# Optimization experiments

Measured on AMD Instinct MI355X. Metric: run time of the kernel, lower is better.

## Reference

```python
import jax, jax.numpy as jnp
import numpy as np

B, N, D = 2, 4096, 2048
H, DH, W = 8, 128, 512          # heads (num_queries), dim_head, window_size
SCALE = 8.0                      # qk_scale (qk_rmsnorm=True)


def setup_inputs() -> dict:
    key = jax.random.key(0)
    ks = jax.random.split(key, 5)
    return {
        "x": jax.random.normal(ks[0], (B, N, D), jnp.float32),
        "Wq": jax.random.normal(ks[1], (H * DH, D), jnp.float32) * 0.02,
        "Wkv": jax.random.normal(ks[2], (2 * H * DH, D), jnp.float32) * 0.02,
        "q_scale": jnp.ones((DH,), jnp.float32),
        "k_scale": jnp.ones((DH,), jnp.float32),
        "Wg": jax.random.normal(ks[3], (H, D), jnp.float32) * 0.02,
        "bg": jnp.zeros((H,), jnp.float32),
        "Wo": jax.random.normal(ks[4], (D, H * DH), jnp.float32) * 0.02,
    }


def _l2norm(t):
    # F.normalize: x / max(||x||, eps)
    return t / jnp.maximum(jnp.linalg.norm(t, axis=-1, keepdims=True), 1e-12)


def reference(x, Wq, Wkv, q_scale, k_scale, Wg, bg, Wo):
    b, n, _ = x.shape
    inner = H * DH
    q = (x @ Wq.T).reshape(b, n, H, DH).transpose(0, 2, 1, 3)      # b h n d
    kv = x @ Wkv.T
    k = kv[..., :inner].reshape(b, n, H, DH).transpose(0, 2, 1, 3)
    v = kv[..., inner:].reshape(b, n, H, DH).transpose(0, 2, 1, 3)
    # qk rmsnorm
    q = _l2norm(q) * q_scale
    k = _l2norm(k) * k_scale

    nb = n // W
    qb = q.reshape(b, H, nb, W, DH)
    kb = k.reshape(b, H, nb, W, DH)
    vb = v.reshape(b, H, nb, W, DH)

    def look_around(t):  # prepend previous bucket (look_backward=1)
        prev = jnp.concatenate([jnp.zeros_like(t[:, :, :1]), t[:, :, :-1]], axis=2)
        return jnp.concatenate([prev, t], axis=3)  # b h nb 2W d

    kw, vw = look_around(kb), look_around(vb)

    pos = jnp.arange(n).reshape(nb, W)
    pos_prev = jnp.concatenate([jnp.full((1, W), -1), pos[:-1]], axis=0)
    posk = jnp.concatenate([pos_prev, pos], axis=1)                 # nb 2W
    dist = pos[:, :, None] - posk[:, None, :]                       # nb W 2W
    # causal + exact window: attend j with 0 <= i - j <= W, valid (non-pad) key
    mask = (posk[:, None, :] >= 0) & (dist >= 0) & (dist <= W)

    sim = jnp.einsum('bhnid,bhnjd->bhnij', qb * SCALE, kw)
    sim = jnp.where(mask, sim, jnp.finfo(sim.dtype).min)
    attn = jax.nn.softmax(sim, axis=-1)
    o = jnp.einsum('bhnij,bhnjd->bhnid', attn, vw).reshape(b, H, n, DH)

    # per-head sigmoid value gating
    gates = jax.nn.sigmoid(jnp.einsum('bnd,hd->bhn', x, Wg) + bg[None, :, None])
    o = o * gates[..., None]

    o = o.transpose(0, 2, 1, 3).reshape(b, n, inner)                # b n (h d)
    return o @ Wo.T
```

## Files before the change

### kernel.cpp

```cpp
#include <hip/hip_runtime.h>
#include <hip/hip_bf16.h>
#include <cstdint>

typedef short short8 __attribute__((ext_vector_type(8)));
typedef __bf16 bf16x8 __attribute__((ext_vector_type(8)));
typedef float f32x4 __attribute__((ext_vector_type(4)));
typedef unsigned short u16;
typedef unsigned int u32;

#define B_  2
#define N_  4096
#define D_  2048
#define H_  8
#define DH_ 128
#define W_  512
#define M_  (B_*N_)
#define INNER_ (H_*DH_)

static __device__ __forceinline__ u16 f2bf(float f) {
  u32 u = __float_as_uint(f);
  u32 r = (u + 0x7fffu + ((u >> 16) & 1u)) >> 16;
  return (u16)r;
}
static __device__ __forceinline__ float bf2f(u16 u) {
  return __uint_as_float(((u32)u) << 16);
}
static __device__ __forceinline__ f32x4 mfma16(short8 a, short8 b, f32x4 c) {
  return __builtin_amdgcn_mfma_f32_16x16x32_bf16(
      __builtin_bit_cast(bf16x8, a), __builtin_bit_cast(bf16x8, b), c, 0, 0, 0);
}

#define GLOAD_LDS16(g, s) \
  __builtin_amdgcn_global_load_lds((const __attribute__((address_space(1))) void*)(g), \
                                   (__attribute__((address_space(3))) void*)(s), 16, 0, 0)

__global__ __launch_bounds__(256) void cvt_kernel(
    const float* __restrict__ x, const float* __restrict__ Wq,
    const float* __restrict__ Wkv, const float* __restrict__ Wo,
    u16* __restrict__ xb, u16* __restrict__ Wcat, u16* __restrict__ Wob) {
  size_t i = ((size_t)blockIdx.x * 256 + threadIdx.x) * 8;
  const float* src; u16* dst; size_t off;
  const size_t SX = 16777216ul, SQ = 2097152ul, SKV = 4194304ul;
  if (i < SX)                { src = x;   dst = xb;             off = i; }
  else if (i < SX+SQ)        { src = Wq;  dst = Wcat;           off = i - SX; }
  else if (i < SX+SQ+SKV)    { src = Wkv; dst = Wcat + 2097152; off = i - SX - SQ; }
  else                       { src = Wo;  dst = Wob;            off = i - SX - SQ - SKV; }
  float4 a = *(const float4*)(src + off);
  float4 b = *(const float4*)(src + off + 4);
  short8 o;
  o[0]=(short)f2bf(a.x); o[1]=(short)f2bf(a.y); o[2]=(short)f2bf(a.z); o[3]=(short)f2bf(a.w);
  o[4]=(short)f2bf(b.x); o[5]=(short)f2bf(b.y); o[6]=(short)f2bf(b.z); o[7]=(short)f2bf(b.w);
  *(short8*)(dst + off) = o;
}

#define BARRIER() __builtin_amdgcn_s_barrier()
#define WAIT_LGKM0() do { asm volatile("s_waitcnt lgkmcnt(0)" ::: "memory"); \
                          __builtin_amdgcn_sched_barrier(0); } while(0)
#define WVM8 asm volatile("s_waitcnt vmcnt(8)" ::: "memory")
#define WVM4 asm volatile("s_waitcnt vmcnt(4)" ::: "memory")
#define WVM0 asm volatile("s_waitcnt vmcnt(0)" ::: "memory")
#define WNONE ((void)0)

#define STAGE_HALF(gbase, sreg) do { \
    const u16* _g = (gbase) + _cs; \
    GLOAD_LDS16(_g + (size_t)(wv*32 + (lane>>2))*K,      (sreg) + wv*1024); \
    GLOAD_LDS16(_g + (size_t)(wv*32 + 16 + (lane>>2))*K, (sreg) + wv*1024 + 512); \
  } while(0)

#define LOAD_AF(sreg, mfb) do { \
    _Pragma("unroll") for (int q = 0; q < 4; ++q) \
      af[q] = *(const short8*)((sreg) + (wm*128 + ((mfb)+q)*16 + l15)*32 + fch); \
  } while(0)
#define LOAD_BF(sreg) do { \
    _Pragma("unroll") for (int q = 0; q < 4; ++q) \
      bf[q] = *(const short8*)((sreg) + (wn*64 + q*16 + l15)*32 + fch); \
  } while(0)

#define PH_MFMA(mfb) do { \
    __builtin_amdgcn_s_setprio(1); \
    _Pragma("unroll") for (int q = 0; q < 4; ++q) \
      _Pragma("unroll") for (int nf = 0; nf < 4; ++nf) \
        acc[(mfb)+q][nf] = mfma16(af[q], bf[nf], acc[(mfb)+q][nf]); \
    __builtin_amdgcn_s_setprio(0); \
  } while(0)

#define TILE4(T, SA_C, SB_C, SA_N, SB_N, C1, C2, WB, WA) do { \
    const u16* gAt = gA + (size_t)(T)*64; \
    const u16* gBt = gB + (size_t)(T)*64; \
    short8 af[4], bf[4]; \
    LOAD_AF(SA_C, 0); LOAD_BF(SB_C); \
    if (C1) STAGE_HALF(gAt + 96, (SA_N) + 8192); \
    BARRIER(); WAIT_LGKM0(); PH_MFMA(0); BARRIER(); \
    LOAD_AF(SA_C, 4); \
    if (C1) STAGE_HALF(gBt + 96, (SB_N) + 8192); \
    WB; \
    BARRIER(); WAIT_LGKM0(); PH_MFMA(4); BARRIER(); \
    LOAD_AF((SA_C) + 8192, 0); LOAD_BF((SB_C) + 8192); \
    if (C2) STAGE_HALF(gAt + 128, SA_C); \
    BARRIER(); WAIT_LGKM0(); PH_MFMA(0); BARRIER(); \
    LOAD_AF((SA_C) + 8192, 4); \
    if (C2) STAGE_HALF(gBt + 128, SB_C); \
    WA; \
    BARRIER(); WAIT_LGKM0(); PH_MFMA(4); BARRIER(); \
  } while(0)

template<int EPI>
__global__ __launch_bounds__(512, 2) void gemm256(
    const u16* __restrict__ A, const u16* __restrict__ Bw,
    u16* __restrict__ Dq, u16* __restrict__ Dk, u16* __restrict__ Dv,
    float* __restrict__ Cf, int Ncols, int K) {
  extern __shared__ u16 lds[];
  const int tid = threadIdx.x;
  const int lane = tid & 63, wv = tid >> 6;
  const int wm = wv >> 2, wn = wv & 3;
  const int l15 = lane & 15, l4 = lane >> 4;

  const int nwg = gridDim.x;
  const int swz = (blockIdx.x & 7) * (nwg >> 3) + (blockIdx.x >> 3);
  const int by = swz & 31;
  const int bx = swz >> 5;
  const int m0 = by << 8, n0 = bx << 8;

  const u16* gA = A + (size_t)m0 * K;
  const u16* gB = Bw + (size_t)n0 * K;
  u16* sA0 = lds;
  u16* sB0 = lds + 32768;

  const int _cs = ((lane & 3) ^ ((lane >> 3) & 3)) * 8;
  const int fch = (l4 ^ ((l15 >> 1) & 3)) * 8;

  f32x4 acc[8][4] = {};

  STAGE_HALF(gA,      sA0);
  STAGE_HALF(gB,      sB0);
  STAGE_HALF(gA + 32, sA0 + 8192);
  STAGE_HALF(gB + 32, sB0 + 8192);
  STAGE_HALF(gA + 64, sA0 + 16384);
  STAGE_HALF(gB + 64, sB0 + 16384);
  WVM4;
  BARRIER();

  const int nt = K >> 6;
  #pragma unroll 1
  for (int t = 0; t < nt - 2; t += 2) {
    TILE4(t,     sA0,         sB0,         sA0 + 16384, sB0 + 16384, true, true, WVM8, WVM8);
    TILE4(t + 1, sA0 + 16384, sB0 + 16384, sA0,         sB0,         true, true, WVM8, WVM8);
  }
  TILE4(nt - 2, sA0,         sB0,         sA0 + 16384, sB0 + 16384, true,  false, WVM8, WVM4);
  TILE4(nt - 1, sA0 + 16384, sB0 + 16384, sA0,         sB0,         false, false, WVM0, WNONE);

  if (EPI == 0) {
    #pragma unroll
    for (int mf = 0; mf < 8; ++mf)
      #pragma unroll
      for (int nf = 0; nf < 4; ++nf)
        #pragma unroll
        for (int j = 0; j < 4; ++j) {
          int m = m0 + wm*128 + mf*16 + l4*4 + j;
          int gc = n0 + wn*64 + nf*16 + l15;
          int bufsel = gc >> 10, inner = gc & 1023, h = inner >> 7, d = inner & 127;
          u16* dst = bufsel == 0 ? Dq : (bufsel == 1 ? Dk : Dv);
          int b = m >> 12, n = m & (N_ - 1);
          dst[(((size_t)(b*H_ + h)*N_ + n) << 7) + d] = f2bf(acc[mf][nf][j]);
        }
  } else {
    #pragma unroll
    for (int mf = 0; mf < 8; ++mf)
      #pragma unroll
      for (int nf = 0; nf < 4; ++nf)
        #pragma unroll
        for (int j = 0; j < 4; ++j) {
          int m = m0 + wm*128 + mf*16 + l4*4 + j;
          int gc = n0 + wn*64 + nf*16 + l15;
          Cf[(size_t)m*Ncols + gc] = acc[mf][nf][j];
        }
  }
}

__global__ __launch_bounds__(256) void normqk_kernel(
    u16* __restrict__ qb, u16* __restrict__ kb,
    const float* __restrict__ qs, const float* __restrict__ ks) {
  int lane = threadIdx.x & 63, wv = threadIdx.x >> 6;
  size_t vec = (size_t)blockIdx.x * 4 + wv;
  bool isq = vec < 65536;
  u16* p = isq ? qb + vec*128 : kb + (vec - 65536)*128;
  const float* sc = isq ? qs : ks;
  u32 u = *(const u32*)(p + lane*2);
  float a = bf2f((u16)(u & 0xffffu));
  float b = bf2f((u16)(u >> 16));
  float ss = a*a + b*b;
  #pragma unroll
  for (int off = 32; off >= 1; off >>= 1) ss += __shfl_xor(ss, off);
  float inv = 1.0f / fmaxf(sqrtf(ss), 1e-12f);
  if (isq) inv *= 8.0f;
  float r0 = a * inv * sc[lane*2];
  float r1 = b * inv * sc[lane*2 + 1];
  *(u32*)(p + lane*2) = (u32)f2bf(r0) | ((u32)f2bf(r1) << 16);
}

__global__ __launch_bounds__(256) void transpose_v_kernel(
    const u16* __restrict__ v, u16* __restrict__ vT) {
  int bh = blockIdx.x >> 6;
  int n0 = (blockIdx.x & 63) << 6;
  __shared__ u16 tl[64][136];
  int tid = threadIdx.x;
  #pragma unroll
  for (int r = 0; r < 4; ++r) {
    int cf = r*256 + tid;
    int row = cf >> 4, ch = cf & 15;
    *(short8*)&tl[row][ch*8] = *(const short8*)(v + ((size_t)bh*N_ + n0 + row)*128 + ch*8);
  }
  __syncthreads();
  #pragma unroll
  for (int r = 0; r < 4; ++r) {
    int cf = r*256 + tid;
    int d = cf >> 3, nch = cf & 7;
    short8 o;
    #pragma unroll
    for (int i = 0; i < 8; ++i) o[i] = (short)tl[nch*8 + i][d];
    *(short8*)(vT + ((size_t)bh*128 + d)*N_ + n0 + nch*8) = o;
  }
}

__global__ __launch_bounds__(256) void gates_kernel(
    const float* __restrict__ x, const float* __restrict__ Wg,
    const float* __restrict__ bg, float* __restrict__ gates) {
  int m = blockIdx.x;
  int tid = threadIdx.x;
  const float* xr = x + (size_t)m * D_;
  float acc[8] = {};
  for (int d = tid; d < D_; d += 256) {
    float xv = xr[d];
    #pragma unroll
    for (int h = 0; h < 8; ++h) acc[h] = fmaf(xv, Wg[h*D_ + d], acc[h]);
  }
  #pragma unroll
  for (int h = 0; h < 8; ++h)
    #pragma unroll
    for (int off = 32; off >= 1; off >>= 1) acc[h] += __shfl_xor(acc[h], off);
  __shared__ float red[4][8];
  int lane = tid & 63, wv = tid >> 6;
  if (lane == 0) {
    #pragma unroll
    for (int h = 0; h < 8; ++h) red[wv][h] = acc[h];
  }
  __syncthreads();
  if (tid < 8) {
    float vsum = red[0][tid] + red[1][tid] + red[2][tid] + red[3][tid] + bg[tid];
    gates[(size_t)m*8 + tid] = 1.0f / (1.0f + __expf(-vsum));
  }
}

__global__ __launch_bounds__(256) void attn_kernel(
    const u16* __restrict__ q, const u16* __restrict__ k,
    const u16* __restrict__ vT, const float* __restrict__ gates,
    u16* __restrict__ o) {
  const int bid = blockIdx.x;
  const int t = bid & 3;
  const int c = (bid >> 2) & 7;
  const int bh = bid >> 5;
  const int b = bh >> 3, h = bh & 7;
  const int i0 = c*W_ + t*128;
  const int tid = threadIdx.x;
  const int lane = tid & 63, wv = tid >> 6;
  const int l15 = lane & 15, l4 = lane >> 4;

  __shared__ u16 sK[64*128];
  __shared__ u16 sV[128*64];
  __shared__ u16 sP[4][32*64];

  short8 qf[2][4];
  const u16* qbase = q + (((size_t)bh*N_ + i0 + wv*32) << 7);
  #pragma unroll
  for (int mf = 0; mf < 2; ++mf)
    #pragma unroll
    for (int ks = 0; ks < 4; ++ks)
      qf[mf][ks] = *(const short8*)(qbase + (mf*16 + l15)*128 + ks*32 + l4*8);

  float mrow[2][4], lrow[2][4];
  f32x4 oacc[2][8];
  #pragma unroll
  for (int mf = 0; mf < 2; ++mf) {
    #pragma unroll
    for (int j = 0; j < 4; ++j) { mrow[mf][j] = -1e30f; lrow[mf][j] = 0.f; }
    #pragma unroll
    for (int df = 0; df < 8; ++df) oacc[mf][df] = (f32x4){0.f,0.f,0.f,0.f};
  }
  u16* sPw = &sP[wv][0];

  #pragma unroll 1
  for (int kt = 0; kt < 10; ++kt) {
    const int j0 = i0 - 512 + kt*64;
    if (j0 < 0) continue;
    __syncthreads();
    #pragma unroll
    for (int r = 0; r < 4; ++r) {
      int cf = r*256 + tid;
      int row = cf >> 4, cph = cf & 15;
      int clg = cph ^ (row & 15);
      GLOAD_LDS16(k + (((size_t)bh*N_ + j0 + row) << 7) + clg*8, sK + (size_t)(r*256 + wv*64)*8);
    }
    #pragma unroll
    for (int r = 0; r < 4; ++r) {
      int cf = r*256 + tid;
      int row = cf >> 3, cph = cf & 7;
      int clg = cph ^ (row & 7);
      GLOAD_LDS16(vT + ((size_t)bh*128 + row)*N_ + j0 + clg*8, sV + (size_t)(r*256 + wv*64)*8);
    }
    __syncthreads();

    f32x4 s[2][4];
    #pragma unroll
    for (int mf = 0; mf < 2; ++mf)
      #pragma unroll
      for (int nf = 0; nf < 4; ++nf) s[mf][nf] = (f32x4){0.f,0.f,0.f,0.f};
    #pragma unroll
    for (int ks = 0; ks < 4; ++ks) {
      short8 kb[4];
      #pragma unroll
      for (int nf = 0; nf < 4; ++nf) {
        int row = nf*16 + l15;
        int ch = (ks*4 + l4) ^ (row & 15);
        kb[nf] = *(const short8*)(sK + row*128 + ch*8);
      }
      #pragma unroll
      for (int mf = 0; mf < 2; ++mf)
        #pragma unroll
        for (int nf = 0; nf < 4; ++nf)
          s[mf][nf] = mfma16(qf[mf][ks], kb[nf], s[mf][nf]);
    }

    if (kt < 2 || kt > 7) {
      #pragma unroll
      for (int mf = 0; mf < 2; ++mf)
        #pragma unroll
        for (int nf = 0; nf < 4; ++nf)
          #pragma unroll
          for (int j = 0; j < 4; ++j) {
            int r = wv*32 + mf*16 + l4*4 + j;
            int sidx = nf*16 + l15;
            int dist = (i0 + r) - (j0 + sidx);
            if (dist < 0 || dist > 512) s[mf][nf][j] = -1e30f;
          }
    }

    #pragma unroll
    for (int mf = 0; mf < 2; ++mf) {
      #pragma unroll
      for (int j = 0; j < 4; ++j) {
        float mx = fmaxf(fmaxf(s[mf][0][j], s[mf][1][j]), fmaxf(s[mf][2][j], s[mf][3][j]));
        #pragma unroll
        for (int off = 1; off <= 8; off <<= 1) mx = fmaxf(mx, __shfl_xor(mx, off));
        float mnew = fmaxf(mrow[mf][j], mx);
        float scal = __expf(mrow[mf][j] - mnew);
        mrow[mf][j] = mnew;
        float ls = 0.f;
        #pragma unroll
        for (int nf = 0; nf < 4; ++nf) {
          float p = __expf(s[mf][nf][j] - mnew);
          s[mf][nf][j] = p;
          ls += p;
        }
        #pragma unroll
        for (int off = 1; off <= 8; off <<= 1) ls += __shfl_xor(ls, off);
        lrow[mf][j] = lrow[mf][j]*scal + ls;
        #pragma unroll
        for (int df = 0; df < 8; ++df) oacc[mf][df][j] *= scal;
        int prow = mf*16 + l4*4 + j;
        #pragma unroll
        for (int nf = 0; nf < 4; ++nf) {
          int pcol = nf*16 + l15;
          int ch = (pcol >> 3) ^ (prow & 7);
          sPw[prow*64 + ch*8 + (pcol & 7)] = f2bf(s[mf][nf][j]);
        }
      }
    }

    #pragma unroll
    for (int ks2 = 0; ks2 < 2; ++ks2) {
      short8 pa[2];
      #pragma unroll
      for (int mf = 0; mf < 2; ++mf) {
        int prow = mf*16 + l15;
        int ch = (ks2*4 + l4) ^ (prow & 7);
        pa[mf] = *(const short8*)(sPw + prow*64 + ch*8);
      }
      #pragma unroll
      for (int df = 0; df < 8; ++df) {
        int vd = df*16 + l15;
        int ch2 = (ks2*4 + l4) ^ (vd & 7);
        short8 vb = *(const short8*)(sV + vd*64 + ch2*8);
        #pragma unroll
        for (int mf = 0; mf < 2; ++mf)
          oacc[mf][df] = mfma16(pa[mf], vb, oacc[mf][df]);
      }
    }
  }

  #pragma unroll
  for (int mf = 0; mf < 2; ++mf)
    #pragma unroll
    for (int j = 0; j < 4; ++j) {
      int r = wv*32 + mf*16 + l4*4 + j;
      int i = i0 + r;
      float f = (1.0f / lrow[mf][j]) * gates[((size_t)b*N_ + i)*8 + h];
      #pragma unroll
      for (int df = 0; df < 8; ++df)
        o[((size_t)b*N_ + i)*INNER_ + h*128 + df*16 + l15] = f2bf(oacc[mf][df][j] * f);
    }
}

extern "C" void kernel_launch(void* const* d_in, const int* in_sizes, int n_in,
                              void* d_out, int out_size, void* d_ws, size_t ws_size,
                              hipStream_t stream) {
  const float* x       = (const float*)d_in[0];
  const float* Wq      = (const float*)d_in[1];
  const float* Wkv     = (const float*)d_in[2];
  const float* q_scale = (const float*)d_in[3];
  const float* k_scale = (const float*)d_in[4];
  const float* Wg      = (const float*)d_in[5];
  const float* bg      = (const float*)d_in[6];
  const float* Wo      = (const float*)d_in[7];
  float* out = (float*)d_out;

  u16* qb  = (u16*)d_out;
  u16* kb  = qb + 8388608;
  u16* vb  = kb + 8388608;
  u16* vTb = vb + 8388608;

  char* w = (char*)d_ws;
  u16* xb   = (u16*)w;
  u16* ob   = (u16*)w;
  u16* Wcat = (u16*)(w + 33554432);
  u16* Wob  = (u16*)(w + 46137344);
  float* gb = (float*)(w + 50331648);
  (void)in_sizes; (void)n_in; (void)out_size; (void)ws_size;

  hipFuncSetAttribute((const void*)gemm256<0>,
                      hipFuncAttributeMaxDynamicSharedMemorySize, 131072);
  hipFuncSetAttribute((const void*)gemm256<1>,
                      hipFuncAttributeMaxDynamicSharedMemorySize, 131072);

  cvt_kernel<<<12288, 256, 0, stream>>>(x, Wq, Wkv, Wo, xb, Wcat, Wob);
  gemm256<0><<<384, 512, 131072, stream>>>(xb, Wcat, qb, kb, vb, nullptr, 3072, 2048);
  normqk_kernel<<<32768, 256, 0, stream>>>(qb, kb, q_scale, k_scale);
  transpose_v_kernel<<<1024, 256, 0, stream>>>(vb, vTb);
  gates_kernel<<<8192, 256, 0, stream>>>(x, Wg, bg, gb);
  attn_kernel<<<512, 256, 0, stream>>>(qb, kb, vTb, gb, ob);
  gemm256<1><<<256, 512, 131072, stream>>>(ob, Wob, nullptr, nullptr, nullptr, out, 2048, 1024);
}
```

Baseline: 311.4 us.

## Double-buffer GEMM LDS fragments in registers and read bf16 x in gates

```diff
diff --git a/kernel.cpp b/kernel.cpp
--- a/kernel.cpp
+++ b/kernel.cpp
@@ -54,9 +54,8 @@
 }
 
 #define BARRIER() __builtin_amdgcn_s_barrier()
-#define WAIT_LGKM0() do { asm volatile("s_waitcnt lgkmcnt(0)" ::: "memory"); \
-                          __builtin_amdgcn_sched_barrier(0); } while(0)
-#define WVM8 asm volatile("s_waitcnt vmcnt(8)" ::: "memory")
+#define SB0 __builtin_amdgcn_sched_barrier(0)
+#define WVM6 asm volatile("s_waitcnt vmcnt(6)" ::: "memory")
 #define WVM4 asm volatile("s_waitcnt vmcnt(4)" ::: "memory")
 #define WVM0 asm volatile("s_waitcnt vmcnt(0)" ::: "memory")
 #define WNONE ((void)0)
@@ -67,41 +66,46 @@
     GLOAD_LDS16(_g + (size_t)(wv*32 + 16 + (lane>>2))*K, (sreg) + wv*1024 + 512); \
   } while(0)
 
-#define LOAD_AF(sreg, mfb) do { \
+#define DSA4(dst, sbase, mfb) do { \
     _Pragma("unroll") for (int q = 0; q < 4; ++q) \
-      af[q] = *(const short8*)((sreg) + (wm*128 + ((mfb)+q)*16 + l15)*32 + fch); \
+      dst[q] = *(const short8*)((sbase) + (wm*128 + ((mfb)+q)*16 + l15)*32 + fch); \
   } while(0)
-#define LOAD_BF(sreg) do { \
+#define DSB4(dst, sbase) do { \
     _Pragma("unroll") for (int q = 0; q < 4; ++q) \
-      bf[q] = *(const short8*)((sreg) + (wn*64 + q*16 + l15)*32 + fch); \
+      dst[q] = *(const short8*)((sbase) + (wn*64 + q*16 + l15)*32 + fch); \
   } while(0)
 
-#define PH_MFMA(mfb) do { \
+#define MM16(afr, bfr, mfb) do { \
     __builtin_amdgcn_s_setprio(1); \
     _Pragma("unroll") for (int q = 0; q < 4; ++q) \
       _Pragma("unroll") for (int nf = 0; nf < 4; ++nf) \
-        acc[(mfb)+q][nf] = mfma16(af[q], bf[nf], acc[(mfb)+q][nf]); \
+        acc[(mfb)+q][nf] = mfma16(afr[q], bfr[nf], acc[(mfb)+q][nf]); \
     __builtin_amdgcn_s_setprio(0); \
   } while(0)
 
-#define TILE4(T, SA_C, SB_C, SA_N, SB_N, C1, C2, WB, WA) do { \
+#define TILE4(T, SA_C, SB_C, SA_N, SB_N, C1, C2, P4, V1, V3) do { \
     const u16* gAt = gA + (size_t)(T)*64; \
     const u16* gBt = gB + (size_t)(T)*64; \
-    short8 af[4], bf[4]; \
-    LOAD_AF(SA_C, 0); LOAD_BF(SB_C); \
+    DSA4(afn, SA_C, 4); \
     if (C1) STAGE_HALF(gAt + 96, (SA_N) + 8192); \
-    BARRIER(); WAIT_LGKM0(); PH_MFMA(0); BARRIER(); \
-    LOAD_AF(SA_C, 4); \
+    SB0; BARRIER(); \
+    MM16(afc, bfc, 0); \
+    V1; BARRIER(); \
+    DSA4(afc, (SA_C) + 8192, 0); DSB4(bfn, (SB_C) + 8192); \
     if (C1) STAGE_HALF(gBt + 96, (SB_N) + 8192); \
-    WB; \
-    BARRIER(); WAIT_LGKM0(); PH_MFMA(4); BARRIER(); \
-    LOAD_AF((SA_C) + 8192, 0); LOAD_BF((SB_C) + 8192); \
+    SB0; BARRIER(); \
+    MM16(afn, bfc, 4); \
+    BARRIER(); \
+    DSA4(afn, (SA_C) + 8192, 4); \
     if (C2) STAGE_HALF(gAt + 128, SA_C); \
-    BARRIER(); WAIT_LGKM0(); PH_MFMA(0); BARRIER(); \
-    LOAD_AF((SA_C) + 8192, 4); \
+    SB0; BARRIER(); \
+    MM16(afc, bfn, 0); \
+    V3; BARRIER(); \
+    if (P4) { DSA4(afc, SA_N, 0); DSB4(bfc, SB_N); } \
     if (C2) STAGE_HALF(gBt + 128, SB_C); \
-    WA; \
-    BARRIER(); WAIT_LGKM0(); PH_MFMA(4); BARRIER(); \
+    SB0; BARRIER(); \
+    MM16(afn, bfn, 4); \
+    BARRIER(); \
   } while(0)
 
 template<int EPI>
@@ -130,6 +134,7 @@
   const int fch = (l4 ^ ((l15 >> 1) & 3)) * 8;
 
   f32x4 acc[8][4] = {};
+  short8 afc[4], afn[4], bfc[4], bfn[4];
 
   STAGE_HALF(gA,      sA0);
   STAGE_HALF(gB,      sB0);
@@ -137,17 +142,19 @@
   STAGE_HALF(gB + 32, sB0 + 8192);
   STAGE_HALF(gA + 64, sA0 + 16384);
   STAGE_HALF(gB + 64, sB0 + 16384);
-  WVM4;
+  asm volatile("s_waitcnt vmcnt(8)" ::: "memory");
   BARRIER();
+  DSA4(afc, sA0, 0); DSB4(bfc, sB0);
+  SB0;
 
   const int nt = K >> 6;
   #pragma unroll 1
   for (int t = 0; t < nt - 2; t += 2) {
-    TILE4(t,     sA0,         sB0,         sA0 + 16384, sB0 + 16384, true, true, WVM8, WVM8);
-    TILE4(t + 1, sA0 + 16384, sB0 + 16384, sA0,         sB0,         true, true, WVM8, WVM8);
-  }
-  TILE4(nt - 2, sA0,         sB0,         sA0 + 16384, sB0 + 16384, true,  false, WVM8, WVM4);
-  TILE4(nt - 1, sA0 + 16384, sB0 + 16384, sA0,         sB0,         false, false, WVM0, WNONE);
+    TILE4(t,     sA0,         sB0,         sA0 + 16384, sB0 + 16384, true, true, true, WVM6, WVM6);
+    TILE4(t + 1, sA0 + 16384, sB0 + 16384, sA0,         sB0,         true, true, true, WVM6, WVM6);
+  }
+  TILE4(nt - 2, sA0,         sB0,         sA0 + 16384, sB0 + 16384, true,  false, true,  WVM6, WVM4);
+  TILE4(nt - 1, sA0 + 16384, sB0 + 16384, sA0,         sB0,         false, false, false, WVM0, WNONE);
 
   if (EPI == 0) {
     #pragma unroll
@@ -223,16 +230,20 @@
 }
 
 __global__ __launch_bounds__(256) void gates_kernel(
-    const float* __restrict__ x, const float* __restrict__ Wg,
+    const u16* __restrict__ xb, const float* __restrict__ Wg,
     const float* __restrict__ bg, float* __restrict__ gates) {
   int m = blockIdx.x;
   int tid = threadIdx.x;
-  const float* xr = x + (size_t)m * D_;
+  const u16* xr = xb + (size_t)m * D_;
   float acc[8] = {};
-  for (int d = tid; d < D_; d += 256) {
-    float xv = xr[d];
-    #pragma unroll
-    for (int h = 0; h < 8; ++h) acc[h] = fmaf(xv, Wg[h*D_ + d], acc[h]);
+  for (int d0 = tid*8; d0 < D_; d0 += 256*8) {
+    short8 xv8 = *(const short8*)(xr + d0);
+    #pragma unroll
+    for (int e = 0; e < 8; ++e) {
+      float xv = bf2f((u16)xv8[e]);
+      #pragma unroll
+      for (int h = 0; h < 8; ++h) acc[h] = fmaf(xv, Wg[h*D_ + d0 + e], acc[h]);
+    }
   }
   #pragma unroll
   for (int h = 0; h < 8; ++h)
@@ -445,7 +456,7 @@
   gemm256<0><<<384, 512, 131072, stream>>>(xb, Wcat, qb, kb, vb, nullptr, 3072, 2048);
   normqk_kernel<<<32768, 256, 0, stream>>>(qb, kb, q_scale, k_scale);
   transpose_v_kernel<<<1024, 256, 0, stream>>>(vb, vTb);
-  gates_kernel<<<8192, 256, 0, stream>>>(x, Wg, bg, gb);
+  gates_kernel<<<8192, 256, 0, stream>>>(xb, Wg, bg, gb);
   attn_kernel<<<512, 256, 0, stream>>>(qb, kb, vTb, gb, ob);
   gemm256<1><<<256, 512, 131072, stream>>>(ob, Wob, nullptr, nullptr, nullptr, out, 2048, 1024);
 }
```

Result: no change. 306.7 us (-1.5%).
